# Kernel optimization log

Hardware: AMD Instinct MI355X
Metric: run time of the kernel (lower is better)

The kernel has to match this reference:

```python
import jax, jax.numpy as jnp
import numpy as np

EPS = 1e-5
NEG = -1000000.0
H = 8

def layer_norm(v, g, b):
    mu = jnp.mean(v, axis=-1, keepdims=True)
    var = jnp.var(v, axis=-1, keepdims=True)
    return (v - mu) * jax.lax.rsqrt(var + EPS) * g + b

def setup_inputs() -> dict:
    key = jax.random.key(0)
    ks = jax.random.split(key, 12)
    B, T, Tc, D, Dc = 8, 2048, 512, 1024, 512
    s = lambda fan: 1.0 / np.sqrt(fan)
    return {
        'query': jax.random.normal(ks[0], (B, T, D), jnp.float32),
        'x': jax.random.normal(ks[1], (B, T, D), jnp.float32),
        'cond_emb': jax.random.normal(ks[2], (B, Tc, Dc), jnp.float32),
        'src_mask': jax.random.uniform(ks[3], (B, T, 1), jnp.float32),
        'cond_mask': jax.random.uniform(ks[4], (B, Tc, 1), jnp.float32),
        'norm_x_g': jnp.ones((D,), jnp.float32),
        'norm_x_b': jnp.zeros((D,), jnp.float32),
        'norm_c_g': jnp.ones((Dc,), jnp.float32),
        'norm_c_b': jnp.zeros((Dc,), jnp.float32),
        'W_kc': jax.random.normal(ks[5], (D, Dc), jnp.float32) * s(Dc),
        'b_kc': jnp.zeros((D,), jnp.float32),
        'W_vc': jax.random.normal(ks[6], (D, Dc), jnp.float32) * s(Dc),
        'b_vc': jnp.zeros((D,), jnp.float32),
        'W_kx': jax.random.normal(ks[7], (D, D), jnp.float32) * s(D),
        'b_kx': jnp.zeros((D,), jnp.float32),
        'W_vx': jax.random.normal(ks[8], (D, D), jnp.float32) * s(D),
        'b_vx': jnp.zeros((D,), jnp.float32),
        'W_y': jax.random.normal(ks[9], (D, D), jnp.float32) * s(D),
        'b_y': jnp.zeros((D,), jnp.float32),
    }

def reference(query, x, cond_emb, src_mask, cond_mask,
              norm_x_g, norm_x_b, norm_c_g, norm_c_b,
              W_kc, b_kc, W_vc, b_vc, W_kx, b_kx, W_vx, b_vx, W_y, b_y):
    B, T, D = x.shape
    Tc = cond_emb.shape[1]
    N = T + Tc
    xn = layer_norm(x, norm_x_g, norm_x_b)          # (B,T,D)
    cn = layer_norm(cond_emb, norm_c_g, norm_c_b)   # (B,Tc,Dc)
    # keys with additive mask penalty, concatenated over sequence dim
    k_cond = cn @ W_kc.T + b_kc + (1.0 - cond_mask) * NEG
    k_x = xn @ W_kx.T + b_kx + (1.0 - src_mask) * NEG
    key = jnp.concatenate([k_cond, k_x], axis=1)    # (B,N,D)
    q = jax.nn.softmax(query.reshape(B, T, H, D // H), axis=-1)
    k = jax.nn.softmax(key.reshape(B, N, H, D // H), axis=1)
    v_cond = (cn @ W_vc.T + b_vc) * cond_mask
    v_x = (xn @ W_vx.T + b_vx) * src_mask
    v = jnp.concatenate([v_cond, v_x], axis=1).reshape(B, N, H, D // H)
    attn = jnp.einsum('bnhd,bnhl->bhdl', k, v)      # (B,H,d,d) linear-attention KV
    y = jnp.einsum('bthd,bhdl->bthl', q, attn).reshape(B, T, D)
    return y @ W_y.T + b_y
```

## Files before the change

kernel.cpp:

```cpp
#include <hip/hip_runtime.h>


typedef short s16x8 __attribute__((ext_vector_type(8)));
typedef float f32x4 __attribute__((ext_vector_type(4)));

__device__ __forceinline__ float b2f(short s) {
    unsigned int u = ((unsigned int)(unsigned short)s) << 16;
    return __uint_as_float(u);
}
__device__ __forceinline__ short f2b(float f) {
    unsigned int u = __float_as_uint(f);
    u += 0x7fffu + ((u >> 16) & 1u);
    return (short)(u >> 16);
}

typedef void __attribute__((address_space(1)))* gas_ptr;
typedef void __attribute__((address_space(3)))* las_ptr;
__device__ __forceinline__ void async_cp16(const void* g, void* l) {
    __builtin_amdgcn_global_load_lds((gas_ptr)g, (las_ptr)l, 16, 0, 0);
}

__device__ __forceinline__ float pen_of(const float* __restrict__ cmask,
                                        const float* __restrict__ smask,
                                        int b, int n) {
    float mk = (n < 512) ? cmask[b * 512 + n] : smask[b * 2048 + n - 512];
    return (1.0f - mk) * -1000000.0f;
}

__global__ __launch_bounds__(256) void cvt_all(const float* __restrict__ Wkc,
                                               const float* __restrict__ Wvc,
                                               const float* __restrict__ Wkx,
                                               const float* __restrict__ Wvx,
                                               const float* __restrict__ Wy,
                                               short* __restrict__ dst) {
    int g = (blockIdx.x * 256 + threadIdx.x) * 4;
    const float* src;
    if (g < 524288)        src = Wkc + g;
    else if (g < 1048576)  src = Wvc + (g - 524288);
    else if (g < 2097152)  src = Wkx + (g - 1048576);
    else if (g < 3145728)  src = Wvx + (g - 2097152);
    else                   src = Wy  + (g - 3145728);
    float4 v = *(const float4*)src;
    short4 o;
    o.x = f2b(v.x); o.y = f2b(v.y); o.z = f2b(v.z); o.w = f2b(v.w);
    *(short4*)&dst[g] = o;
}

__global__ __launch_bounds__(256) void ln_kernel(const float* __restrict__ x,
                                                 const float* __restrict__ g,
                                                 const float* __restrict__ be,
                                                 short* __restrict__ out, int L) {
    long row = blockIdx.x;
    const float* xr = x + row * L;
    short* orow = out + row * L;
    int tid = threadIdx.x;
    int i0 = tid * 4;
    bool active = i0 < L;
    float v0 = 0.f, v1 = 0.f, v2 = 0.f, v3 = 0.f;
    if (active) {
        float4 p = *(const float4*)&xr[i0];
        v0 = p.x; v1 = p.y; v2 = p.z; v3 = p.w;
    }
    float s = v0 + v1 + v2 + v3;
    float s2 = v0*v0 + v1*v1 + v2*v2 + v3*v3;
    #pragma unroll
    for (int off = 32; off > 0; off >>= 1) {
        s  += __shfl_down(s, off);
        s2 += __shfl_down(s2, off);
    }
    __shared__ float ss[4], sq[4];
    int wave = tid >> 6, lane = tid & 63;
    if (lane == 0) { ss[wave] = s; sq[wave] = s2; }
    __syncthreads();
    if (tid == 0) {
        float t1 = ss[0] + ss[1] + ss[2] + ss[3];
        float t2 = sq[0] + sq[1] + sq[2] + sq[3];
        float mu = t1 / (float)L;
        float var = t2 / (float)L - mu * mu;
        ss[0] = mu;
        sq[0] = rsqrtf(var + 1e-5f);
    }
    __syncthreads();
    float mu = ss[0], rs = sq[0];
    if (active) {
        float4 gp = *(const float4*)&g[i0];
        float4 bp = *(const float4*)&be[i0];
        short4 o;
        o.x = f2b((v0 - mu) * rs * gp.x + bp.x);
        o.y = f2b((v1 - mu) * rs * gp.y + bp.y);
        o.z = f2b((v2 - mu) * rs * gp.z + bp.z);
        o.w = f2b((v3 - mu) * rs * gp.w + bp.w);
        *(short4*)&orow[i0] = o;
    }
}

__global__ __launch_bounds__(256) void qsoftmax_kernel(const float* __restrict__ q,
                                                       short* __restrict__ out) {
    long row = (long)blockIdx.x * 4 + (threadIdx.x >> 6);
    int lane = threadIdx.x & 63;
    const float* qr = q + row * 128;
    float2 p = *(const float2*)&qr[lane * 2];
    float v0 = p.x, v1 = p.y;
    float m = fmaxf(v0, v1);
    #pragma unroll
    for (int off = 32; off > 0; off >>= 1) m = fmaxf(m, __shfl_xor(m, off));
    float e0 = __expf(v0 - m), e1 = __expf(v1 - m);
    float s = e0 + e1;
    #pragma unroll
    for (int off = 32; off > 0; off >>= 1) s += __shfl_xor(s, off);
    float inv = 1.0f / s;
    short2 o; o.x = f2b(e0 * inv); o.y = f2b(e1 * inv);
    *(short2*)&out[row * 128 + lane * 2] = o;
}

__global__ __launch_bounds__(256) void kstats1(const short* __restrict__ klog,
                                               const float* __restrict__ cmask,
                                               const float* __restrict__ smask,
                                               float* __restrict__ partM,
                                               float* __restrict__ partS) {
    int c = blockIdx.x * 256 + threadIdx.x;
    int b = blockIdx.y;
    int n0 = blockIdx.z * 256;
    const short* base = klog + (long)b * 2560 * 1024 + c;
    float m = -3.4e38f, s = 0.f;
    for (int k = 0; k < 256; ++k) {
        int n = n0 + k;
        float v = b2f(base[(long)n * 1024]) + pen_of(cmask, smask, b, n);
        float nm = fmaxf(m, v);
        s = s * __expf(m - nm) + __expf(v - nm);
        m = nm;
    }
    long o = ((long)(b * 10 + blockIdx.z)) * 1024 + c;
    partM[o] = m;
    partS[o] = s;
}

__global__ __launch_bounds__(256) void kstats2(const float* __restrict__ partM,
                                               const float* __restrict__ partS,
                                               float* __restrict__ Ms,
                                               float* __restrict__ iSs) {
    int c = blockIdx.x * 256 + threadIdx.x;
    int b = blockIdx.y;
    float M = -3.4e38f;
    #pragma unroll
    for (int k = 0; k < 10; ++k)
        M = fmaxf(M, partM[((long)(b * 10 + k)) * 1024 + c]);
    float S = 0.f;
    #pragma unroll
    for (int k = 0; k < 10; ++k) {
        long o = ((long)(b * 10 + k)) * 1024 + c;
        S += partS[o] * __expf(partM[o] - M);
    }
    Ms[b * 1024 + c] = M;
    iSs[b * 1024 + c] = 1.0f / S;
}

template<int MODE>
__global__ __launch_bounds__(256) void gemm_bt(
        const short* __restrict__ A, int lda, long strideA,
        const short* __restrict__ B, int ldb,
        void* __restrict__ OutA, void* __restrict__ OutB,
        int ldo, long strideO,
        int K,
        const float* __restrict__ biasK, const float* __restrict__ biasV,
        const float* __restrict__ mask, long strideMask) {
    __shared__ short As[128 * 64];
    __shared__ short Bs[128 * 64];
    int tid = threadIdx.x;
    int wave = tid >> 6, lane = tid & 63;
    int n0 = blockIdx.x * 128;
    int m0 = blockIdx.y * 128;
    int z = blockIdx.z;

    const short* Ab;
    const short* Bb;
    if (MODE == 2) {
        Ab = A + (z & 7) * 128;
        Bb = B + (long)z * 16384;
    } else if (MODE == 4) {
        Ab = A + (long)z * strideA;
        Bb = B + (long)z * 1048576;
    } else {
        Ab = A + (long)z * strideA;
        Bb = B;
    }

    f32x4 acc[4][4];
    #pragma unroll
    for (int i = 0; i < 4; ++i)
        #pragma unroll
        for (int j = 0; j < 4; ++j) {
            f32x4 zz = {0.f, 0.f, 0.f, 0.f};
            acc[i][j] = zz;
        }

    int wm = wave >> 1, wn = wave & 1;
    int r = lane & 15, q = lane >> 4;

    for (int k0 = 0; k0 < K; k0 += 64) {
        __syncthreads();
        #pragma unroll
        for (int it = 0; it < 4; ++it) {
            int cid = it * 256 + tid;
            int row = cid >> 3;
            int c8  = cid & 7;
            int col = ((c8 ^ (row & 7)) << 3);
            const short* ga = Ab + (long)(m0 + row) * lda + k0 + col;
            const short* gb = Bb + (long)(n0 + row) * ldb + k0 + col;
            async_cp16(ga, &As[cid * 8]);
            async_cp16(gb, &Bs[cid * 8]);
        }
        __syncthreads();
        #pragma unroll
        for (int kk = 0; kk < 64; kk += 32) {
            s16x8 af[4], bfr[4];
            #pragma unroll
            for (int i = 0; i < 4; ++i) {
                int rowA = wm * 64 + i * 16 + r;
                int rowB = wn * 64 + i * 16 + r;
                int ch = (kk >> 3) + q;
                af[i]  = *(const s16x8*)&As[rowA * 64 + ((ch ^ (rowA & 7)) << 3)];
                bfr[i] = *(const s16x8*)&Bs[rowB * 64 + ((ch ^ (rowB & 7)) << 3)];
            }
            #pragma unroll
            for (int i = 0; i < 4; ++i)
                #pragma unroll
                for (int j = 0; j < 4; ++j)
                    acc[i][j] = __builtin_amdgcn_mfma_f32_16x16x32_bf16(af[i], bfr[j], acc[i][j], 0, 0, 0);
        }
    }

    #pragma unroll
    for (int i = 0; i < 4; ++i) {
        int gmb = m0 + wm * 64 + i * 16 + q * 4;
        #pragma unroll
        for (int j = 0; j < 4; ++j) {
            int gn = n0 + wn * 64 + j * 16 + r;
            #pragma unroll
            for (int rg = 0; rg < 4; ++rg) {
                int row = gmb + rg;
                float v = acc[i][j][rg];
                if (MODE == 0) {
                    if (gn < 1024) {
                        ((short*)OutA)[(long)z * strideO + (long)row * ldo + gn] =
                            f2b(v + biasK[gn]);
                    } else {
                        int gv = gn - 1024;
                        float mk = mask[(long)z * strideMask + row];
                        ((short*)OutB)[(long)z * strideO + (long)row * ldo + gv] =
                            f2b((v + biasV[gv]) * mk);
                    }
                } else if (MODE == 2) {
                    ((short*)OutA)[(long)(z >> 3) * 1048576 + (long)row * 1024 +
                                   (z & 7) * 128 + gn] = f2b(v);
                } else {
                    ((float*)OutA)[(long)z * strideO + (long)row * ldo + gn] =
                        v + biasK[gn];
                }
            }
        }
    }
}

__global__ __launch_bounds__(256) void attn_part(const short* __restrict__ klog,
                                                 const short* __restrict__ vbuf,
                                                 const float* __restrict__ cmask,
                                                 const float* __restrict__ smask,
                                                 const float* __restrict__ Ms,
                                                 float* __restrict__ pbuf) {
    __shared__ short kT[128 * 64];
    __shared__ short vT[128 * 64];
    int ns = blockIdx.x;
    int z = blockIdx.y;
    int b = z >> 3, h = z & 7;
    int tid = threadIdx.x;
    int wave = tid >> 6, lane = tid & 63;
    int r = lane & 15, q = lane >> 4;
    int wm = wave >> 1, wn = wave & 1;

    int cg = h * 128 + lane * 2;
    float M0 = Ms[b * 1024 + cg];
    float M1 = Ms[b * 1024 + cg + 1];

    f32x4 acc[4][4];
    #pragma unroll
    for (int i = 0; i < 4; ++i)
        #pragma unroll
        for (int j = 0; j < 4; ++j) {
            f32x4 zz = {0.f, 0.f, 0.f, 0.f};
            acc[i][j] = zz;
        }

    long base = ((long)b * 2560) * 1024 + h * 128;
    int nbase = ns * 320;
    int swz = (lane & 7) << 3;
    for (int n0 = 0; n0 < 320; n0 += 64) {
        __syncthreads();
        #pragma unroll 4
        for (int i = 0; i < 16; ++i) {
            int nl = i * 4 + wave;
            int n = nbase + n0 + nl;
            float pen = pen_of(cmask, smask, b, n);
            long g = base + (long)n * 1024 + lane * 2;
            short2 k2 = *(const short2*)&klog[g];
            short2 v2 = *(const short2*)&vbuf[g];
            float w0 = __expf(b2f(k2.x) + pen - M0);
            float w1 = __expf(b2f(k2.y) + pen - M1);
            int c = lane * 2;
            int sw = nl ^ swz;
            kT[c * 64 + sw] = f2b(w0);
            kT[(c + 1) * 64 + sw] = f2b(w1);
            vT[c * 64 + sw] = v2.x;
            vT[(c + 1) * 64 + sw] = v2.y;
        }
        __syncthreads();
        #pragma unroll
        for (int kk = 0; kk < 64; kk += 32) {
            s16x8 af[4], bfr[4];
            #pragma unroll
            for (int i = 0; i < 4; ++i) {
                int cA = wm * 64 + i * 16 + r;
                int cB = wn * 64 + i * 16 + r;
                af[i]  = *(const s16x8*)&kT[cA * 64 + ((kk + q * 8) ^ (((cA >> 1) & 7) << 3))];
                bfr[i] = *(const s16x8*)&vT[cB * 64 + ((kk + q * 8) ^ (((cB >> 1) & 7) << 3))];
            }
            #pragma unroll
            for (int i = 0; i < 4; ++i)
                #pragma unroll
                for (int j = 0; j < 4; ++j)
                    acc[i][j] = __builtin_amdgcn_mfma_f32_16x16x32_bf16(af[i], bfr[j], acc[i][j], 0, 0, 0);
        }
    }
    float* outp = pbuf + ((long)z * 8 + ns) * 16384;
    #pragma unroll
    for (int i = 0; i < 4; ++i) {
        int d0 = wm * 64 + i * 16 + q * 4;
        #pragma unroll
        for (int j = 0; j < 4; ++j) {
            int l = wn * 64 + j * 16 + r;
            *(f32x4*)&outp[l * 128 + d0] = acc[i][j];
        }
    }
}

__global__ __launch_bounds__(256) void reduce_attn(const float* __restrict__ pbuf,
                                                   const float* __restrict__ iSs,
                                                   short* __restrict__ attnD) {
    int idx = blockIdx.x * 256 + threadIdx.x;
    int z = idx >> 14, rem = idx & 16383;
    int d = rem & 127, l = rem >> 7;
    int b = z >> 3, h = z & 7;
    const float* p = pbuf + (long)z * 8 * 16384 + rem;
    float s = 0.f;
    #pragma unroll
    for (int ns = 0; ns < 8; ++ns) s += p[ns * 16384];
    attnD[(long)z * 16384 + d * 128 + l] = f2b(s * iSs[b * 1024 + h * 128 + d]);
}

extern "C" void kernel_launch(void* const* d_in, const int* in_sizes, int n_in,
                              void* d_out, int out_size, void* d_ws, size_t ws_size,
                              hipStream_t stream) {
    const float* query = (const float*)d_in[0];
    const float* x     = (const float*)d_in[1];
    const float* cond  = (const float*)d_in[2];
    const float* smask = (const float*)d_in[3];
    const float* cmask = (const float*)d_in[4];
    const float* gx  = (const float*)d_in[5];
    const float* bx  = (const float*)d_in[6];
    const float* gc  = (const float*)d_in[7];
    const float* bc  = (const float*)d_in[8];
    const float* Wkc = (const float*)d_in[9];
    const float* bkc = (const float*)d_in[10];
    const float* Wvc = (const float*)d_in[11];
    const float* bvc = (const float*)d_in[12];
    const float* Wkx = (const float*)d_in[13];
    const float* bkx = (const float*)d_in[14];
    const float* Wvx = (const float*)d_in[15];
    const float* bvx = (const float*)d_in[16];
    const float* Wy  = (const float*)d_in[17];
    const float* by  = (const float*)d_in[18];

    size_t o_xn    = 0;
    size_t o_cn    = o_xn    + 33554432;
    size_t o_klog  = o_cn    + 4194304;
    size_t o_vbuf  = o_klog  + 41943040;
    size_t o_qsm   = o_vbuf  + 41943040;
    size_t o_attnD = o_qsm   + 33554432;
    size_t o_partM = o_attnD + 2097152;
    size_t o_partS = o_partM + 327680;
    size_t o_Ms    = o_partS + 327680;
    size_t o_iSs   = o_Ms    + 32768;
    size_t o_wkc   = o_iSs   + 32768;
    size_t o_wvc   = o_wkc   + 1048576;
    size_t o_wkx   = o_wvc   + 1048576;
    size_t o_wvx   = o_wkx   + 2097152;
    size_t o_wy    = o_wvx   + 2097152;
    size_t need    = o_wy    + 2097152;
    if (ws_size < need) return;

    char* w = (char*)d_ws;
    short* xn    = (short*)(w + o_xn);
    short* cn    = (short*)(w + o_cn);
    short* klog  = (short*)(w + o_klog);
    short* vbuf  = (short*)(w + o_vbuf);
    short* qsm   = (short*)(w + o_qsm);
    short* attnD = (short*)(w + o_attnD);
    float* partM = (float*)(w + o_partM);
    float* partS = (float*)(w + o_partS);
    float* Ms    = (float*)(w + o_Ms);
    float* iSs   = (float*)(w + o_iSs);
    short* wkc   = (short*)(w + o_wkc);
    short* wkx   = (short*)(w + o_wkx);
    short* wy    = (short*)(w + o_wy);
    float* pbuf  = (float*)xn;
    short* Zt    = klog;

    cvt_all<<<4096, 256, 0, stream>>>(Wkc, Wvc, Wkx, Wvx, Wy, wkc);

    ln_kernel<<<16384, 256, 0, stream>>>(x, gx, bx, xn, 1024);
    ln_kernel<<<4096, 256, 0, stream>>>(cond, gc, bc, cn, 512);
    qsoftmax_kernel<<<32768, 256, 0, stream>>>(query, qsm);

    gemm_bt<0><<<dim3(16, 16, 8), 256, 0, stream>>>(
        xn, 1024, 2097152L, wkx, 1024,
        klog + 512 * 1024, vbuf + 512 * 1024, 1024, 2621440L,
        1024, bkx, bvx, smask, 2048L);
    gemm_bt<0><<<dim3(16, 4, 8), 256, 0, stream>>>(
        cn, 512, 262144L, wkc, 512,
        klog, vbuf, 1024, 2621440L,
        512, bkc, bvc, cmask, 512L);

    kstats1<<<dim3(4, 8, 10), 256, 0, stream>>>(klog, cmask, smask, partM, partS);
    kstats2<<<dim3(4, 8), 256, 0, stream>>>(partM, partS, Ms, iSs);

    attn_part<<<dim3(8, 64), 256, 0, stream>>>(klog, vbuf, cmask, smask, Ms, pbuf);
    reduce_attn<<<4096, 256, 0, stream>>>(pbuf, iSs, attnD);

    gemm_bt<2><<<dim3(1, 8, 64), 256, 0, stream>>>(
        wy, 1024, 0L, attnD, 128,
        Zt, nullptr, 1024, 0L,
        128, nullptr, nullptr, nullptr, 0L);
    gemm_bt<4><<<dim3(8, 16, 8), 256, 0, stream>>>(
        qsm, 1024, 2097152L, Zt, 1024,
        d_out, nullptr, 1024, 2097152L,
        1024, by, nullptr, nullptr, 0L);
}
```

Before: 535.1 us.

## Add 256x256-tile 512-thread GEMM for the two large projections

Adds a new gemm256 kernel using 256x256 output tiles, 8 waves, a 64-wide K step, double-buffered async global-to-LDS loads with XOR swizzle, and 128KB dynamic shared memory. It replaces the previous GEMM for the x key/value projection and the final q·Z output GEMM. The larger tiles raise arithmetic intensity per LDS byte and cut global reloads. In exchange the grid shrinks (512 and 256 blocks), which may underfill 256 CUs, and register pressure from 32 accumulators per thread may limit occupancy.

```diff
diff --git a/kernel.cpp b/kernel.cpp
--- a/kernel.cpp
+++ b/kernel.cpp
@@ -253,6 +253,126 @@
                 } else if (MODE == 2) {
                     ((short*)OutA)[(long)(z >> 3) * 1048576 + (long)row * 1024 +
                                    (z & 7) * 128 + gn] = f2b(v);
+                } else {
+                    ((float*)OutA)[(long)z * strideO + (long)row * ldo + gn] =
+                        v + biasK[gn];
+                }
+            }
+        }
+    }
+}
+
+template<int MODE>
+__global__ __launch_bounds__(512, 2) void gemm256(
+        const short* __restrict__ A, int lda, long strideA,
+        const short* __restrict__ B, int ldb,
+        void* __restrict__ OutA, void* __restrict__ OutB,
+        int ldo, long strideO,
+        int K,
+        const float* __restrict__ biasK, const float* __restrict__ biasV,
+        const float* __restrict__ mask, long strideMask) {
+    extern __shared__ short lds[];
+    int tid = threadIdx.x;
+    int wave = tid >> 6, lane = tid & 63;
+    int n0 = blockIdx.x * 256;
+    int m0 = blockIdx.y * 256;
+    int z = blockIdx.z;
+
+    const short* Ab;
+    const short* Bb;
+    if (MODE == 4) {
+        Ab = A + (long)z * strideA;
+        Bb = B + (long)z * 1048576;
+    } else {
+        Ab = A + (long)z * strideA;
+        Bb = B;
+    }
+
+    f32x4 acc[8][4];
+    #pragma unroll
+    for (int i = 0; i < 8; ++i)
+        #pragma unroll
+        for (int j = 0; j < 4; ++j) {
+            f32x4 zz = {0.f, 0.f, 0.f, 0.f};
+            acc[i][j] = zz;
+        }
+
+    int wm = wave >> 2, wn = wave & 3;
+    int r = lane & 15, q = lane >> 4;
+
+    auto stage = [&](int buf, int k0) {
+        short* dstb = lds + buf * 32768;
+        #pragma unroll
+        for (int it = 0; it < 8; ++it) {
+            int cid = it * 512 + tid;
+            int rid = cid & 2047;
+            int row = rid >> 3;
+            int c8  = rid & 7;
+            int col = ((c8 ^ (row & 7)) << 3);
+            const short* g = (cid < 2048)
+                ? (Ab + (long)(m0 + row) * lda + k0 + col)
+                : (Bb + (long)(n0 + row) * ldb + k0 + col);
+            async_cp16(g, dstb + cid * 8);
+        }
+    };
+
+    auto compute = [&](int buf) {
+        const short* Asb = lds + buf * 32768;
+        const short* Bsb = Asb + 16384;
+        s16x8 bfr[2][4];
+        #pragma unroll
+        for (int kk2 = 0; kk2 < 2; ++kk2)
+            #pragma unroll
+            for (int j = 0; j < 4; ++j) {
+                int rowB = wn * 64 + j * 16 + r;
+                int ch = kk2 * 4 + q;
+                bfr[kk2][j] = *(const s16x8*)&Bsb[rowB * 64 + ((ch ^ (rowB & 7)) << 3)];
+            }
+        __builtin_amdgcn_s_setprio(1);
+        #pragma unroll
+        for (int i = 0; i < 8; ++i) {
+            int rowA = wm * 128 + i * 16 + r;
+            s16x8 a0 = *(const s16x8*)&Asb[rowA * 64 + (((q    ) ^ (rowA & 7)) << 3)];
+            s16x8 a1 = *(const s16x8*)&Asb[rowA * 64 + (((q + 4) ^ (rowA & 7)) << 3)];
+            #pragma unroll
+            for (int j = 0; j < 4; ++j)
+                acc[i][j] = __builtin_amdgcn_mfma_f32_16x16x32_bf16(a0, bfr[0][j], acc[i][j], 0, 0, 0);
+            #pragma unroll
+            for (int j = 0; j < 4; ++j)
+                acc[i][j] = __builtin_amdgcn_mfma_f32_16x16x32_bf16(a1, bfr[1][j], acc[i][j], 0, 0, 0);
+        }
+        __builtin_amdgcn_s_setprio(0);
+    };
+
+    int nt = K >> 6;
+    stage(0, 0);
+    __syncthreads();
+    for (int t = 0; t < nt; ++t) {
+        if (t + 1 < nt) stage((t + 1) & 1, (t + 1) << 6);
+        compute(t & 1);
+        __syncthreads();
+    }
+
+    #pragma unroll
+    for (int i = 0; i < 8; ++i) {
+        int gmb = m0 + wm * 128 + i * 16 + q * 4;
+        #pragma unroll
+        for (int j = 0; j < 4; ++j) {
+            int gn = n0 + wn * 64 + j * 16 + r;
+            #pragma unroll
+            for (int rg = 0; rg < 4; ++rg) {
+                int row = gmb + rg;
+                float v = acc[i][j][rg];
+                if (MODE == 0) {
+                    if (gn < 1024) {
+                        ((short*)OutA)[(long)z * strideO + (long)row * ldo + gn] =
+                            f2b(v + biasK[gn]);
+                    } else {
+                        int gv = gn - 1024;
+                        float mk = mask[(long)z * strideMask + row];
+                        ((short*)OutB)[(long)z * strideO + (long)row * ldo + gv] =
+                            f2b((v + biasV[gv]) * mk);
+                    }
                 } else {
                     ((float*)OutA)[(long)z * strideO + (long)row * ldo + gn] =
                         v + biasK[gn];
@@ -415,13 +535,22 @@
     float* pbuf  = (float*)xn;
     short* Zt    = klog;
 
+    static bool attr_set = false;
+    if (!attr_set) {
+        (void)hipFuncSetAttribute((const void*)gemm256<0>,
+                                  hipFuncAttributeMaxDynamicSharedMemorySize, 131072);
+        (void)hipFuncSetAttribute((const void*)gemm256<4>,
+                                  hipFuncAttributeMaxDynamicSharedMemorySize, 131072);
+        attr_set = true;
+    }
+
     cvt_all<<<4096, 256, 0, stream>>>(Wkc, Wvc, Wkx, Wvx, Wy, wkc);
 
     ln_kernel<<<16384, 256, 0, stream>>>(x, gx, bx, xn, 1024);
     ln_kernel<<<4096, 256, 0, stream>>>(cond, gc, bc, cn, 512);
     qsoftmax_kernel<<<32768, 256, 0, stream>>>(query, qsm);
 
-    gemm_bt<0><<<dim3(16, 16, 8), 256, 0, stream>>>(
+    gemm256<0><<<dim3(8, 8, 8), 512, 131072, stream>>>(
         xn, 1024, 2097152L, wkx, 1024,
         klog + 512 * 1024, vbuf + 512 * 1024, 1024, 2621440L,
         1024, bkx, bvx, smask, 2048L);
@@ -440,7 +569,7 @@
         wy, 1024, 0L, attnD, 128,
         Zt, nullptr, 1024, 0L,
         128, nullptr, nullptr, nullptr, 0L);
-    gemm_bt<4><<<dim3(8, 16, 8), 256, 0, stream>>>(
+    gemm256<4><<<dim3(4, 8, 8), 512, 131072, stream>>>(
         qsm, 1024, 2097152L, Zt, 1024,
         d_out, nullptr, 1024, 2097152L,
         1024, by, nullptr, nullptr, 0L);
```

Result: faster. 500.0 us (-6.6%).

## Pipeline GEMM K-loop with 4-stage async LDS buffers and XCD-aware block remap

Applied to the files above, without the earlier changes.

Reworks the bf16 GEMM main loop into a 4-buffer ring of 32-wide K tiles. Loads run three stages ahead using async global-to-LDS copies, with explicit vmcnt waits and a single barrier per step, and the MFMA block is raised in wave priority. The LDS layout is repacked so two rows share a 64-element swizzled line. Block indices are also remapped so that neighbouring tiles land on the same XCD, to improve L2 reuse. The aim is to hide global load latency and halve the barriers per K step, at the cost of 64KB of LDS per block (lower occupancy) and a remap that assumes gridDim.y*gridDim.z is divisible by 8.

```diff
diff --git a/kernel.cpp b/kernel.cpp
--- a/kernel.cpp
+++ b/kernel.cpp
@@ -25,6 +25,17 @@
                                         int b, int n) {
     float mk = (n < 512) ? cmask[b * 512 + n] : smask[b * 2048 + n - 512];
     return (1.0f - mk) * -1000000.0f;
+}
+
+__device__ __forceinline__ void xcd_remap(int& gx, int& gy, int& gz) {
+    int lb = blockIdx.x + gridDim.x * (blockIdx.y + gridDim.y * blockIdx.z);
+    int nx = gridDim.x;
+    int gpx = (gridDim.y * gridDim.z) >> 3;
+    int xcd = lb & 7, rest = lb >> 3;
+    gx = rest % nx;
+    int gidx = xcd * gpx + rest / nx;
+    gy = gidx % gridDim.y;
+    gz = gidx / gridDim.y;
 }
 
 __global__ __launch_bounds__(256) void cvt_all(const float* __restrict__ Wkc,
@@ -164,13 +175,14 @@
         int K,
         const float* __restrict__ biasK, const float* __restrict__ biasV,
         const float* __restrict__ mask, long strideMask) {
-    __shared__ short As[128 * 64];
-    __shared__ short Bs[128 * 64];
+    __shared__ short lds[4 * 8192];
     int tid = threadIdx.x;
     int wave = tid >> 6, lane = tid & 63;
-    int n0 = blockIdx.x * 128;
-    int m0 = blockIdx.y * 128;
-    int z = blockIdx.z;
+    int bx, by, bz;
+    xcd_remap(bx, by, bz);
+    int n0 = bx * 128;
+    int m0 = by * 128;
+    int z = bz;
 
     const short* Ab;
     const short* Bb;
@@ -197,37 +209,79 @@
     int wm = wave >> 1, wn = wave & 1;
     int r = lane & 15, q = lane >> 4;
 
-    for (int k0 = 0; k0 < K; k0 += 64) {
-        __syncthreads();
+    const short* sp0; const short* sp1; const short* sp2; const short* sp3;
+    int lo0, lo1, lo2, lo3;
+    {
         #pragma unroll
         for (int it = 0; it < 4; ++it) {
             int cid = it * 256 + tid;
-            int row = cid >> 3;
-            int c8  = cid & 7;
-            int col = ((c8 ^ (row & 7)) << 3);
-            const short* ga = Ab + (long)(m0 + row) * lda + k0 + col;
-            const short* gb = Bb + (long)(n0 + row) * ldb + k0 + col;
-            async_cp16(ga, &As[cid * 8]);
-            async_cp16(gb, &Bs[cid * 8]);
-        }
-        __syncthreads();
-        #pragma unroll
-        for (int kk = 0; kk < 64; kk += 32) {
-            s16x8 af[4], bfr[4];
+            int rid = cid & 511;
+            int srow = rid >> 3;
+            int scol = rid & 7;
+            int scol0 = scol ^ (srow & 7);
+            int row = srow * 2 + (scol0 >> 2);
+            int col = (scol0 & 3) << 3;
+            const short* p = (cid < 512)
+                ? (Ab + (long)(m0 + row) * lda + col)
+                : (Bb + (long)(n0 + row) * ldb + col);
+            int lo = cid * 8;
+            if (it == 0) { sp0 = p; lo0 = lo; }
+            else if (it == 1) { sp1 = p; lo1 = lo; }
+            else if (it == 2) { sp2 = p; lo2 = lo; }
+            else { sp3 = p; lo3 = lo; }
+        }
+    }
+
+    int offA[4], offB[4];
+    #pragma unroll
+    for (int i = 0; i < 4; ++i) {
+        int rowA = wm * 64 + i * 16 + r;
+        int srow = rowA >> 1;
+        int slot = ((((rowA & 1) << 2) | q) ^ (srow & 7));
+        offA[i] = srow * 64 + slot * 8;
+        int rowB = wn * 64 + i * 16 + r;
+        int srowB = rowB >> 1;
+        int slotB = ((((rowB & 1) << 2) | q) ^ (srowB & 7));
+        offB[i] = 4096 + srowB * 64 + slotB * 8;
+    }
+
+    int nt = K >> 5;
+    #pragma unroll
+    for (int pt = 0; pt < 3; ++pt) {
+        async_cp16(sp0 + (pt << 5), &lds[pt * 8192 + lo0]);
+        async_cp16(sp1 + (pt << 5), &lds[pt * 8192 + lo1]);
+        async_cp16(sp2 + (pt << 5), &lds[pt * 8192 + lo2]);
+        async_cp16(sp3 + (pt << 5), &lds[pt * 8192 + lo3]);
+    }
+
+    for (int t = 0; t < nt; ++t) {
+        if (t + 2 < nt)
+            asm volatile("s_waitcnt vmcnt(8)\n\ts_barrier" ::: "memory");
+        else if (t + 1 < nt)
+            asm volatile("s_waitcnt vmcnt(4)\n\ts_barrier" ::: "memory");
+        else
+            asm volatile("s_waitcnt vmcnt(0)\n\ts_barrier" ::: "memory");
+        const short* base = &lds[(t & 3) * 8192];
+        s16x8 af[4], bfr[4];
+        #pragma unroll
+        for (int j = 0; j < 4; ++j) bfr[j] = *(const s16x8*)&base[offB[j]];
+        #pragma unroll
+        for (int i = 0; i < 4; ++i) af[i] = *(const s16x8*)&base[offA[i]];
+        if (t + 3 < nt) {
+            int buf = (t + 3) & 3;
+            int ks = (t + 3) << 5;
+            async_cp16(sp0 + ks, &lds[buf * 8192 + lo0]);
+            async_cp16(sp1 + ks, &lds[buf * 8192 + lo1]);
+            async_cp16(sp2 + ks, &lds[buf * 8192 + lo2]);
+            async_cp16(sp3 + ks, &lds[buf * 8192 + lo3]);
+        }
+        __builtin_amdgcn_s_setprio(1);
+        #pragma unroll
+        for (int i = 0; i < 4; ++i)
             #pragma unroll
-            for (int i = 0; i < 4; ++i) {
-                int rowA = wm * 64 + i * 16 + r;
-                int rowB = wn * 64 + i * 16 + r;
-                int ch = (kk >> 3) + q;
-                af[i]  = *(const s16x8*)&As[rowA * 64 + ((ch ^ (rowA & 7)) << 3)];
-                bfr[i] = *(const s16x8*)&Bs[rowB * 64 + ((ch ^ (rowB & 7)) << 3)];
-            }
-            #pragma unroll
-            for (int i = 0; i < 4; ++i)
-                #pragma unroll
-                for (int j = 0; j < 4; ++j)
-                    acc[i][j] = __builtin_amdgcn_mfma_f32_16x16x32_bf16(af[i], bfr[j], acc[i][j], 0, 0, 0);
-        }
+            for (int j = 0; j < 4; ++j)
+                acc[i][j] = __builtin_amdgcn_mfma_f32_16x16x32_bf16(af[i], bfr[j], acc[i][j], 0, 0, 0);
+        __builtin_amdgcn_s_setprio(0);
     }
 
     #pragma unroll
```

Measured after the change: 514.5 us. 3.8% less time.
